# Performance work log

Hardware: AMD Instinct MI355X
Metric: run time of the kernel (lower is better)

## Reference

```python
import jax, jax.numpy as jnp
import numpy as np

EPS = 1e-5
NUM_C, NUM_D = 16, 32


def setup_inputs() -> dict:
    key = jax.random.key(0)
    k1, k2 = jax.random.split(key)
    x = jax.random.normal(k1, (64, NUM_C * NUM_D, 32, 32), dtype=jnp.float32)
    # grouped 1x1 conv weight: per-capsule D_out x D_in matrix (torch init copies identity)
    eye = jnp.broadcast_to(jnp.eye(NUM_D, dtype=jnp.float32), (NUM_C, NUM_D, NUM_D))
    weight = eye + 0.02 * jax.random.normal(k2, (NUM_C, NUM_D, NUM_D), dtype=jnp.float32)
    bias = jnp.zeros((NUM_C * NUM_D,), dtype=jnp.float32)
    return {"x": x, "weight": weight, "bias": bias}


def reference(x, weight, bias):
    N, CD, H, W = x.shape
    C = weight.shape[0]
    D = CD // C
    # BatchNorm2d (training mode, affine=False): biased variance over (N, H, W)
    mean = jnp.mean(x, axis=(0, 2, 3), keepdims=True)
    var = jnp.mean(jnp.square(x - mean), axis=(0, 2, 3), keepdims=True)
    xn = (x - mean) * jax.lax.rsqrt(var + EPS)
    # grouped 1x1 conv == per-capsule DxD matmul
    xg = xn.reshape(N, C, D, H, W)
    out = jnp.einsum('ncihw,coi->ncohw', xg, weight)
    out = out.reshape(N, CD, H, W) + bias[None, :, None, None]
    return out
```

## Files before the change

### kernel.cpp

```cpp
#include <hip/hip_runtime.h>


#define NELEM_PER_CH 65536.0f

__global__ __launch_bounds__(256) void caps_stats(const float* __restrict__ x,
                                                  float* __restrict__ ws) {
    const int ch = blockIdx.x;
    const int tid = threadIdx.x;
    const float4* __restrict__ x4 = (const float4*)x;

    float s = 0.f, ss = 0.f;
#pragma unroll 4
    for (int n = 0; n < 64; ++n) {
        float4 v = x4[((size_t)n * 512 + ch) * 256 + tid];
        s  += v.x + v.y + v.z + v.w;
        ss += v.x * v.x + v.y * v.y + v.z * v.z + v.w * v.w;
    }

#pragma unroll
    for (int off = 32; off > 0; off >>= 1) {
        s  += __shfl_down(s, off);
        ss += __shfl_down(ss, off);
    }
    __shared__ float red[4][2];
    const int wid = tid >> 6;
    if ((tid & 63) == 0) { red[wid][0] = s; red[wid][1] = ss; }
    __syncthreads();
    if (tid == 0) {
        float S = 0.f, SS = 0.f;
#pragma unroll
        for (int w = 0; w < 4; ++w) { S += red[w][0]; SS += red[w][1]; }
        float mean = S / NELEM_PER_CH;
        float var = SS / NELEM_PER_CH - mean * mean;
        ws[ch] = mean;
        ws[512 + ch] = rsqrtf(var + 1e-5f);
    }
}

__global__ __launch_bounds__(1024) void caps_fold(const float* __restrict__ w,
                                                  const float* __restrict__ bias,
                                                  float* __restrict__ ws) {
    const int c = blockIdx.x;
    const int t = threadIdx.x;
    const int o = t >> 5;
    const int i = t & 31;

    const float mean = ws[c * 32 + i];
    const float rstd = ws[512 + c * 32 + i];
    const float wv = w[c * 1024 + t] * rstd;
    ws[1024 + c * 1024 + t] = wv;

    float prod = wv * mean;
#pragma unroll
    for (int off = 16; off > 0; off >>= 1) prod += __shfl_xor(prod, off);
    if (i == 0) ws[17408 + c * 32 + o] = bias[c * 32 + o] - prod;
}

__global__ __launch_bounds__(256) void caps_main(const float* __restrict__ x,
                                                 const float* __restrict__ ws,
                                                 float* __restrict__ out) {
    const int hw = blockIdx.x * 256 + threadIdx.x;
    const int c = blockIdx.y;
    const int n = blockIdx.z;

    const size_t base = (((size_t)n * 16 + c) * 32) * 1024 + hw;
    const float* __restrict__ Wc = ws + 1024 + c * 1024;
    const float* __restrict__ b2 = ws + 17408 + c * 32;

    float xv[32];
#pragma unroll
    for (int i = 0; i < 32; ++i) xv[i] = x[base + (size_t)i * 1024];

#pragma unroll 4
    for (int o = 0; o < 32; ++o) {
        const float* __restrict__ wr = Wc + o * 32;
        float p0 = 0.f, p1 = 0.f, p2 = 0.f, p3 = 0.f;
#pragma unroll
        for (int i = 0; i < 32; i += 4) {
            p0 += wr[i + 0] * xv[i + 0];
            p1 += wr[i + 1] * xv[i + 1];
            p2 += wr[i + 2] * xv[i + 2];
            p3 += wr[i + 3] * xv[i + 3];
        }
        const float r = b2[o] + ((p0 + p1) + (p2 + p3));
        __builtin_nontemporal_store(r, out + base + (size_t)o * 1024);
    }
}

extern "C" void kernel_launch(void* const* d_in, const int* in_sizes, int n_in,
                              void* d_out, int out_size, void* d_ws, size_t ws_size,
                              hipStream_t stream) {
    const float* x    = (const float*)d_in[0];
    const float* w    = (const float*)d_in[1];
    const float* bias = (const float*)d_in[2];
    float* out = (float*)d_out;
    float* ws  = (float*)d_ws;

    caps_stats<<<512, 256, 0, stream>>>(x, ws);
    caps_fold<<<16, 1024, 0, stream>>>(w, bias, ws);
    caps_main<<<dim3(4, 16, 64), 256, 0, stream>>>(x, ws, out);
}
```

Baseline: 74.83 us.

## Process four HW chunks per block with register double-buffered prefetch

The main kernel's grid drops from 4096 to 1024 blocks, and each block now loops over four 256-element spatial chunks of a (n, c) tile. The loads for the next chunk are issued into a second register array before the current chunk's matmul and stores, so memory latency can overlap with compute. The extra 32-float buffer raises register pressure, which can lower occupancy. The smaller grid also gives the GPU fewer waves to hide latency with.

```diff
diff --git a/kernel.cpp b/kernel.cpp
--- a/kernel.cpp
+++ b/kernel.cpp
@@ -2,6 +2,8 @@
 
 
 #define NELEM_PER_CH 65536.0f
+#define WS_WP   1024
+#define WS_BP   17408
 
 __global__ __launch_bounds__(256) void caps_stats(const float* __restrict__ x,
                                                   float* __restrict__ ws) {
@@ -16,20 +18,18 @@
         s  += v.x + v.y + v.z + v.w;
         ss += v.x * v.x + v.y * v.y + v.z * v.z + v.w * v.w;
     }
-
 #pragma unroll
     for (int off = 32; off > 0; off >>= 1) {
         s  += __shfl_down(s, off);
         ss += __shfl_down(ss, off);
     }
     __shared__ float red[4][2];
-    const int wid = tid >> 6;
-    if ((tid & 63) == 0) { red[wid][0] = s; red[wid][1] = ss; }
+    if ((tid & 63) == 0) { red[tid >> 6][0] = s; red[tid >> 6][1] = ss; }
     __syncthreads();
     if (tid == 0) {
         float S = 0.f, SS = 0.f;
 #pragma unroll
-        for (int w = 0; w < 4; ++w) { S += red[w][0]; SS += red[w][1]; }
+        for (int k = 0; k < 4; ++k) { S += red[k][0]; SS += red[k][1]; }
         float mean = S / NELEM_PER_CH;
         float var = SS / NELEM_PER_CH - mean * mean;
         ws[ch] = mean;
@@ -44,46 +44,60 @@
     const int t = threadIdx.x;
     const int o = t >> 5;
     const int i = t & 31;
-
     const float mean = ws[c * 32 + i];
     const float rstd = ws[512 + c * 32 + i];
     const float wv = w[c * 1024 + t] * rstd;
-    ws[1024 + c * 1024 + t] = wv;
-
+    ws[WS_WP + c * 1024 + t] = wv;
     float prod = wv * mean;
 #pragma unroll
     for (int off = 16; off > 0; off >>= 1) prod += __shfl_xor(prod, off);
-    if (i == 0) ws[17408 + c * 32 + o] = bias[c * 32 + o] - prod;
+    if (i == 0) ws[WS_BP + c * 32 + o] = bias[c * 32 + o] - prod;
 }
 
 __global__ __launch_bounds__(256) void caps_main(const float* __restrict__ x,
                                                  const float* __restrict__ ws,
                                                  float* __restrict__ out) {
-    const int hw = blockIdx.x * 256 + threadIdx.x;
-    const int c = blockIdx.y;
-    const int n = blockIdx.z;
+    const int c = blockIdx.x;
+    const int n = blockIdx.y;
+    const int t = threadIdx.x;
 
-    const size_t base = (((size_t)n * 16 + c) * 32) * 1024 + hw;
-    const float* __restrict__ Wc = ws + 1024 + c * 1024;
-    const float* __restrict__ b2 = ws + 17408 + c * 32;
+    const size_t tile = (((size_t)n * 16 + c) * 32) * 1024;
+    const float* __restrict__ xt = x + tile + t;
+    float* __restrict__ ot = out + tile + t;
+    const float* __restrict__ Wc = ws + WS_WP + c * 1024;
+    const float* __restrict__ b2 = ws + WS_BP + c * 32;
 
-    float xv[32];
+    float xv[32], xn[32];
 #pragma unroll
-    for (int i = 0; i < 32; ++i) xv[i] = x[base + (size_t)i * 1024];
+    for (int i = 0; i < 32; ++i) xv[i] = xt[(size_t)i * 1024];
 
+    for (int q = 0; q < 4; ++q) {
+        if (q < 3) {
+#pragma unroll
+            for (int i = 0; i < 32; ++i)
+                xn[i] = xt[(size_t)i * 1024 + (q + 1) * 256];
+        }
+
+        const size_t obase = (size_t)q * 256;
 #pragma unroll 4
-    for (int o = 0; o < 32; ++o) {
-        const float* __restrict__ wr = Wc + o * 32;
-        float p0 = 0.f, p1 = 0.f, p2 = 0.f, p3 = 0.f;
+        for (int o = 0; o < 32; ++o) {
+            const float* __restrict__ wr = Wc + o * 32;
+            float p0 = 0.f, p1 = 0.f, p2 = 0.f, p3 = 0.f;
 #pragma unroll
-        for (int i = 0; i < 32; i += 4) {
-            p0 += wr[i + 0] * xv[i + 0];
-            p1 += wr[i + 1] * xv[i + 1];
-            p2 += wr[i + 2] * xv[i + 2];
-            p3 += wr[i + 3] * xv[i + 3];
+            for (int i = 0; i < 32; i += 4) {
+                p0 += wr[i + 0] * xv[i + 0];
+                p1 += wr[i + 1] * xv[i + 1];
+                p2 += wr[i + 2] * xv[i + 2];
+                p3 += wr[i + 3] * xv[i + 3];
+            }
+            __builtin_nontemporal_store(b2[o] + ((p0 + p1) + (p2 + p3)),
+                                        ot + obase + (size_t)o * 1024);
         }
-        const float r = b2[o] + ((p0 + p1) + (p2 + p3));
-        __builtin_nontemporal_store(r, out + base + (size_t)o * 1024);
+
+        if (q < 3) {
+#pragma unroll
+            for (int i = 0; i < 32; ++i) xv[i] = xn[i];
+        }
     }
 }
 
@@ -98,5 +112,5 @@
 
     caps_stats<<<512, 256, 0, stream>>>(x, ws);
     caps_fold<<<16, 1024, 0, stream>>>(w, bias, ws);
-    caps_main<<<dim3(4, 16, 64), 256, 0, stream>>>(x, ws, out);
+    caps_main<<<dim3(16, 64), 256, 0, stream>>>(x, ws, out);
 }
```

New measurement: 79.59 us. 1.06x slower.

## Fuse stats, fold and apply kernels into one launch with per-capsule spin barriers

Applied to the files above, without the earlier changes.

Merges the three kernels into a single grid: the first 512 blocks compute per-channel mean/rstd and signal a per-capsule counter with release atomics, while the remaining blocks spin-wait on their capsule's counter and then apply normalization inline before the matmul. This drops the separate fold kernel and launch gaps, and lets the apply blocks for early capsules start while other stats blocks are still running. It relies on the stats blocks being scheduled ahead of the waiting blocks (no forward-progress guarantee beyond a spin cap). It also adds an extra init kernel and per-element normalize work in the main loop.

```diff
diff --git a/kernel.cpp b/kernel.cpp
--- a/kernel.cpp
+++ b/kernel.cpp
@@ -2,79 +2,93 @@
 
 
 #define NELEM_PER_CH 65536.0f
+#define WS_CNT 17920
 
-__global__ __launch_bounds__(256) void caps_stats(const float* __restrict__ x,
-                                                  float* __restrict__ ws) {
-    const int ch = blockIdx.x;
-    const int tid = threadIdx.x;
-    const float4* __restrict__ x4 = (const float4*)x;
+__global__ void bar_init(int* __restrict__ cnt) {
+    if (threadIdx.x < 16) cnt[threadIdx.x] = 0;
+}
 
-    float s = 0.f, ss = 0.f;
+__global__ __launch_bounds__(256) void caps_fused(const float* __restrict__ x,
+                                                  const float* __restrict__ w,
+                                                  const float* __restrict__ bias,
+                                                  float* __restrict__ out,
+                                                  float* __restrict__ ws,
+                                                  int* __restrict__ cnt) {
+    const int b = blockIdx.x;
+    const int t = threadIdx.x;
+
+    __shared__ float red[4][2];
+    __shared__ float smean[32], srstd[32];
+
+    if (b < 512) {
+        const int ch = b;
+        const float4* __restrict__ x4 = (const float4*)x;
+        float s = 0.f, ss = 0.f;
 #pragma unroll 4
-    for (int n = 0; n < 64; ++n) {
-        float4 v = x4[((size_t)n * 512 + ch) * 256 + tid];
-        s  += v.x + v.y + v.z + v.w;
-        ss += v.x * v.x + v.y * v.y + v.z * v.z + v.w * v.w;
+        for (int n = 0; n < 64; ++n) {
+            float4 v = x4[((size_t)n * 512 + ch) * 256 + t];
+            s  += v.x + v.y + v.z + v.w;
+            ss += v.x * v.x + v.y * v.y + v.z * v.z + v.w * v.w;
+        }
+#pragma unroll
+        for (int off = 32; off > 0; off >>= 1) {
+            s  += __shfl_down(s, off);
+            ss += __shfl_down(ss, off);
+        }
+        if ((t & 63) == 0) { red[t >> 6][0] = s; red[t >> 6][1] = ss; }
+        __syncthreads();
+        if (t == 0) {
+            float S = 0.f, SS = 0.f;
+#pragma unroll
+            for (int k = 0; k < 4; ++k) { S += red[k][0]; SS += red[k][1]; }
+            const float mean = S / NELEM_PER_CH;
+            const float rstd = rsqrtf(SS / NELEM_PER_CH - mean * mean + 1e-5f);
+            __hip_atomic_store(&ws[ch], mean, __ATOMIC_RELAXED,
+                               __HIP_MEMORY_SCOPE_AGENT);
+            __hip_atomic_store(&ws[512 + ch], rstd, __ATOMIC_RELAXED,
+                               __HIP_MEMORY_SCOPE_AGENT);
+            __hip_atomic_fetch_add(&cnt[ch >> 5], 1, __ATOMIC_RELEASE,
+                                   __HIP_MEMORY_SCOPE_AGENT);
+        }
+        return;
     }
 
-#pragma unroll
-    for (int off = 32; off > 0; off >>= 1) {
-        s  += __shfl_down(s, off);
-        ss += __shfl_down(ss, off);
+    const int m = b - 512;
+    const int c = m >> 8;
+    const int n = (m >> 2) & 63;
+    const int q = m & 3;
+
+    if (t == 0) {
+        int spins = 0;
+        while (__hip_atomic_load(&cnt[c], __ATOMIC_ACQUIRE,
+                                 __HIP_MEMORY_SCOPE_AGENT) < 32 &&
+               spins < (1 << 20)) {
+            ++spins;
+            __builtin_amdgcn_s_sleep(16);
+        }
     }
-    __shared__ float red[4][2];
-    const int wid = tid >> 6;
-    if ((tid & 63) == 0) { red[wid][0] = s; red[wid][1] = ss; }
     __syncthreads();
-    if (tid == 0) {
-        float S = 0.f, SS = 0.f;
-#pragma unroll
-        for (int w = 0; w < 4; ++w) { S += red[w][0]; SS += red[w][1]; }
-        float mean = S / NELEM_PER_CH;
-        float var = SS / NELEM_PER_CH - mean * mean;
-        ws[ch] = mean;
-        ws[512 + ch] = rsqrtf(var + 1e-5f);
+    if (t < 32) {
+        smean[t] = __hip_atomic_load(&ws[c * 32 + t], __ATOMIC_RELAXED,
+                                     __HIP_MEMORY_SCOPE_AGENT);
+        srstd[t] = __hip_atomic_load(&ws[512 + c * 32 + t], __ATOMIC_RELAXED,
+                                     __HIP_MEMORY_SCOPE_AGENT);
     }
-}
+    __syncthreads();
 
-__global__ __launch_bounds__(1024) void caps_fold(const float* __restrict__ w,
-                                                  const float* __restrict__ bias,
-                                                  float* __restrict__ ws) {
-    const int c = blockIdx.x;
-    const int t = threadIdx.x;
-    const int o = t >> 5;
-    const int i = t & 31;
-
-    const float mean = ws[c * 32 + i];
-    const float rstd = ws[512 + c * 32 + i];
-    const float wv = w[c * 1024 + t] * rstd;
-    ws[1024 + c * 1024 + t] = wv;
-
-    float prod = wv * mean;
-#pragma unroll
-    for (int off = 16; off > 0; off >>= 1) prod += __shfl_xor(prod, off);
-    if (i == 0) ws[17408 + c * 32 + o] = bias[c * 32 + o] - prod;
-}
-
-__global__ __launch_bounds__(256) void caps_main(const float* __restrict__ x,
-                                                 const float* __restrict__ ws,
-                                                 float* __restrict__ out) {
-    const int hw = blockIdx.x * 256 + threadIdx.x;
-    const int c = blockIdx.y;
-    const int n = blockIdx.z;
-
-    const size_t base = (((size_t)n * 16 + c) * 32) * 1024 + hw;
-    const float* __restrict__ Wc = ws + 1024 + c * 1024;
-    const float* __restrict__ b2 = ws + 17408 + c * 32;
+    const size_t base = (((size_t)n * 16 + c) * 32) * 1024 + q * 256 + t;
+    const float* __restrict__ Wc = w + c * 1024;
+    const float* __restrict__ bp = bias + c * 32;
 
     float xv[32];
 #pragma unroll
-    for (int i = 0; i < 32; ++i) xv[i] = x[base + (size_t)i * 1024];
+    for (int i = 0; i < 32; ++i)
+        xv[i] = (x[base + (size_t)i * 1024] - smean[i]) * srstd[i];
 
 #pragma unroll 4
     for (int o = 0; o < 32; ++o) {
         const float* __restrict__ wr = Wc + o * 32;
-        float p0 = 0.f, p1 = 0.f, p2 = 0.f, p3 = 0.f;
+        float p0 = bp[o], p1 = 0.f, p2 = 0.f, p3 = 0.f;
 #pragma unroll
         for (int i = 0; i < 32; i += 4) {
             p0 += wr[i + 0] * xv[i + 0];
@@ -82,8 +96,8 @@
             p2 += wr[i + 2] * xv[i + 2];
             p3 += wr[i + 3] * xv[i + 3];
         }
-        const float r = b2[o] + ((p0 + p1) + (p2 + p3));
-        __builtin_nontemporal_store(r, out + base + (size_t)o * 1024);
+        __builtin_nontemporal_store(((p0 + p1) + (p2 + p3)),
+                                    out + base + (size_t)o * 1024);
     }
 }
 
@@ -95,8 +109,8 @@
     const float* bias = (const float*)d_in[2];
     float* out = (float*)d_out;
     float* ws  = (float*)d_ws;
+    int* cnt   = (int*)(ws + WS_CNT);
 
-    caps_stats<<<512, 256, 0, stream>>>(x, ws);
-    caps_fold<<<16, 1024, 0, stream>>>(w, bias, ws);
-    caps_main<<<dim3(4, 16, 64), 256, 0, stream>>>(x, ws, out);
+    bar_init<<<1, 64, 0, stream>>>(cnt);
+    caps_fused<<<512 + 4096, 256, 0, stream>>>(x, w, bias, out, ws, cnt);
 }
```

Result: slower. 282.7 us (+277.7%).
